# Optimization experiments

Hardware: AMD Instinct MI355X
Metric: run time of the kernel (lower is better)

The kernel has to match this reference:

```python
import jax, jax.numpy as jnp
import numpy as np

EMBED_DIM = 1024
NUM_HEADS = 16
HEAD_DIM = EMBED_DIM // NUM_HEADS


def setup_inputs() -> dict:
    key = jax.random.key(0)
    ks = jax.random.split(key, 9)
    B, T, D = 4, 2048, EMBED_DIM
    s = 1.0 / np.sqrt(D)
    inp = {
        "x": jax.random.normal(ks[0], (B, T, D), dtype=jnp.float32),
        "Wq": jax.random.normal(ks[1], (D, D), dtype=jnp.float32) * s,
        "bq": jnp.zeros((D,), dtype=jnp.float32),
        "Wk": jax.random.normal(ks[2], (D, D), dtype=jnp.float32) * s,
        "bk": jnp.zeros((D,), dtype=jnp.float32),
        "Wv": jax.random.normal(ks[3], (D, D), dtype=jnp.float32) * s,
        "bv": jnp.zeros((D,), dtype=jnp.float32),
        "Wo": jax.random.normal(ks[4], (D, D), dtype=jnp.float32) * s,
        "bo": jnp.zeros((D,), dtype=jnp.float32),
    }
    return inp


def _attn(x, Wq, bq, Wk, bk, Wv, bv, Wo, bo):
    B, T, D = x.shape
    H, Hd = NUM_HEADS, HEAD_DIM
    # projections: Linear uses y = x @ W^T + b; here W stored as (D, D) acting as W^T already
    q = (x @ Wq + bq).reshape(B, T, H, Hd).transpose(0, 2, 1, 3)  # [B,H,T,Hd]
    k = (x @ Wk + bk).reshape(B, T, H, Hd).transpose(0, 2, 1, 3)
    v = (x @ Wv + bv).reshape(B, T, H, Hd).transpose(0, 2, 1, 3)
    scores = jnp.einsum("bhqd,bhkd->bhqk", q, k) / np.sqrt(Hd)  # [B,H,T,T]
    causal = jnp.tril(jnp.ones((T, T), dtype=bool))
    scores = jnp.where(causal, scores, -jnp.inf)
    w = jax.nn.softmax(scores, axis=-1)
    out = jnp.einsum("bhqk,bhkd->bhqd", w, v)  # [B,H,T,Hd]
    out = out.transpose(0, 2, 1, 3).reshape(B, T, D)
    return out @ Wo + bo


def reference(x, Wq, bq, Wk, bk, Wv, bv, Wo, bo):
    return _attn(x, Wq, bq, Wk, bk, Wv, bv, Wo, bo)
```

## Files before the change

### kernel.cpp

```cpp
#include <hip/hip_runtime.h>
#include <cstdint>
#include <cstddef>

#define DI __device__ __forceinline__

typedef unsigned short u16;
typedef short bf16x8 __attribute__((ext_vector_type(8)));
typedef unsigned short u16x8 __attribute__((ext_vector_type(8)));
typedef float f32x4 __attribute__((ext_vector_type(4)));

static constexpr int DMODEL = 1024, T = 2048, BB = 4, NH = 16, HD = 64;
static constexpr int M = BB * T;

static constexpr size_t XB_OFF = 0;
static constexpr size_t WT_OFF = (size_t)M * DMODEL;
static constexpr size_t Q_OFF  = WT_OFF + 4ull * DMODEL * DMODEL;
static constexpr size_t K_OFF  = Q_OFF + (size_t)M * DMODEL;
static constexpr size_t V_OFF  = K_OFF + (size_t)M * DMODEL;
static constexpr size_t O_OFF  = XB_OFF;

DI u16 f2bf(float x) {
  unsigned int u = __builtin_bit_cast(unsigned int, x);
  u += 0x7fffu + ((u >> 16) & 1u);
  return (u16)(u >> 16);
}

DI unsigned int cvtpk_bf16(float a, float b) {
  unsigned int r;
  asm("v_cvt_pk_bf16_f32 %0, %1, %2" : "=v"(r) : "v"(a), "v"(b));
  return r;
}

DI void gld_lds16(const void* g, void* l) {
  __builtin_amdgcn_global_load_lds(
      (const __attribute__((address_space(1))) void*)g,
      (__attribute__((address_space(3))) void*)l, 16, 0, 0);
}

__global__ void k_cast(const float* __restrict__ in, u16* __restrict__ out) {
  size_t i = (size_t)(blockIdx.x * 256 + threadIdx.x) * 8;
  float4 a = *(const float4*)(in + i);
  float4 b = *(const float4*)(in + i + 4);
  u16x8 v;
  v[0] = f2bf(a.x); v[1] = f2bf(a.y); v[2] = f2bf(a.z); v[3] = f2bf(a.w);
  v[4] = f2bf(b.x); v[5] = f2bf(b.y); v[6] = f2bf(b.z); v[7] = f2bf(b.w);
  *(u16x8*)(out + i) = v;
}

__global__ void k_transw(const float* __restrict__ Wq, const float* __restrict__ Wk,
                         const float* __restrict__ Wv, const float* __restrict__ Wo,
                         u16* __restrict__ WtBase) {
  __shared__ u16 tile[32][33];
  const int z = blockIdx.z;
  const float* W = z == 0 ? Wq : (z == 1 ? Wk : (z == 2 ? Wv : Wo));
  u16* Wt = WtBase + (size_t)z * DMODEL * DMODEL;
  int tx = threadIdx.x, ty = threadIdx.y;
  int c = blockIdx.x * 32 + tx;
#pragma unroll
  for (int i = 0; i < 4; ++i) {
    int r = blockIdx.y * 32 + ty + i * 8;
    tile[ty + i * 8][tx] = f2bf(W[(size_t)r * DMODEL + c]);
  }
  __syncthreads();
#pragma unroll
  for (int i = 0; i < 4; ++i) {
    int rw = blockIdx.x * 32 + ty + i * 8;
    Wt[(size_t)rw * DMODEL + blockIdx.y * 32 + tx] = tile[tx][ty + i * 8];
  }
}

__launch_bounds__(256, 2)
__global__ void k_gemm_qkv(const u16* __restrict__ A, const u16* __restrict__ Wt,
                           const float* __restrict__ bq, const float* __restrict__ bk,
                           const float* __restrict__ bv,
                           u16* __restrict__ Qo, u16* __restrict__ Ko, u16* __restrict__ Vo) {
  __shared__ u16 As[128 * 64];
  __shared__ u16 Bs[128 * 64];
  const int z = blockIdx.z;
  const u16* Bt = Wt + (size_t)z * DMODEL * DMODEL;
  const float* bias = z == 0 ? bq : (z == 1 ? bk : bv);
  u16* out = z == 0 ? Qo : (z == 1 ? Ko : Vo);
  const float scale = z == 0 ? 0.125f * 1.4426950408889634f : 1.0f;

  const int tid = threadIdx.x;
  const int wave = tid >> 6, lane = tid & 63;
  const int g = lane >> 4, l15 = lane & 15;
  const int brow = blockIdx.x * 128, bcol = blockIdx.y * 128;
  const int wr = wave >> 1, wc = wave & 1;
  const int srow = tid >> 3, schunk = tid & 7;

  f32x4 acc[4][4] = {};

  for (int k0 = 0; k0 < DMODEL; k0 += 64) {
    __syncthreads();
#pragma unroll
    for (int j = 0; j < 4; ++j) {
      int r = j * 32 + srow;
      int cs = (schunk ^ (r & 7)) * 8;
      gld_lds16(A + (size_t)(brow + r) * DMODEL + k0 + cs, (char*)As + j * 4096 + wave * 1024);
      gld_lds16(Bt + (size_t)(bcol + r) * DMODEL + k0 + cs, (char*)Bs + j * 4096 + wave * 1024);
    }
    __syncthreads();
#pragma unroll
    for (int kh = 0; kh < 2; ++kh) {
      bf16x8 af[4], bfr[4];
#pragma unroll
      for (int m = 0; m < 4; ++m) {
        int r = wr * 64 + m * 16 + l15;
        int ch = (kh * 4 + g) ^ (r & 7);
        af[m] = *(const bf16x8*)((const char*)As + r * 128 + ch * 16);
      }
#pragma unroll
      for (int n = 0; n < 4; ++n) {
        int r = wc * 64 + n * 16 + l15;
        int ch = (kh * 4 + g) ^ (r & 7);
        bfr[n] = *(const bf16x8*)((const char*)Bs + r * 128 + ch * 16);
      }
#pragma unroll
      for (int m = 0; m < 4; ++m)
#pragma unroll
        for (int n = 0; n < 4; ++n)
          acc[m][n] = __builtin_amdgcn_mfma_f32_16x16x32_bf16(af[m], bfr[n], acc[m][n], 0, 0, 0);
    }
  }

#pragma unroll
  for (int m = 0; m < 4; ++m)
#pragma unroll
    for (int n = 0; n < 4; ++n) {
      int col = bcol + wc * 64 + n * 16 + l15;
      float bias_v = bias[col];
      int h = col >> 6, d = col & 63;
#pragma unroll
      for (int r = 0; r < 4; ++r) {
        int row = brow + wr * 64 + m * 16 + g * 4 + r;
        int b = row >> 11, t = row & 2047;
        float v = (acc[m][n][r] + bias_v) * scale;
        out[(((size_t)(b * NH + h) * T + t) << 6) + d] = f2bf(v);
      }
    }
}

__launch_bounds__(256, 2)
__global__ void k_gemm_out(const u16* __restrict__ A, const u16* __restrict__ Bt,
                           const float* __restrict__ bias, float* __restrict__ out) {
  __shared__ u16 As[128 * 64];
  __shared__ u16 Bs[128 * 64];
  const int tid = threadIdx.x;
  const int wave = tid >> 6, lane = tid & 63;
  const int g = lane >> 4, l15 = lane & 15;
  const int brow = blockIdx.x * 128, bcol = blockIdx.y * 128;
  const int wr = wave >> 1, wc = wave & 1;
  const int srow = tid >> 3, schunk = tid & 7;

  f32x4 acc[4][4] = {};

  for (int k0 = 0; k0 < DMODEL; k0 += 64) {
    __syncthreads();
#pragma unroll
    for (int j = 0; j < 4; ++j) {
      int r = j * 32 + srow;
      int cs = (schunk ^ (r & 7)) * 8;
      gld_lds16(A + (size_t)(brow + r) * DMODEL + k0 + cs, (char*)As + j * 4096 + wave * 1024);
      gld_lds16(Bt + (size_t)(bcol + r) * DMODEL + k0 + cs, (char*)Bs + j * 4096 + wave * 1024);
    }
    __syncthreads();
#pragma unroll
    for (int kh = 0; kh < 2; ++kh) {
      bf16x8 af[4], bfr[4];
#pragma unroll
      for (int m = 0; m < 4; ++m) {
        int r = wr * 64 + m * 16 + l15;
        int ch = (kh * 4 + g) ^ (r & 7);
        af[m] = *(const bf16x8*)((const char*)As + r * 128 + ch * 16);
      }
#pragma unroll
      for (int n = 0; n < 4; ++n) {
        int r = wc * 64 + n * 16 + l15;
        int ch = (kh * 4 + g) ^ (r & 7);
        bfr[n] = *(const bf16x8*)((const char*)Bs + r * 128 + ch * 16);
      }
#pragma unroll
      for (int m = 0; m < 4; ++m)
#pragma unroll
        for (int n = 0; n < 4; ++n)
          acc[m][n] = __builtin_amdgcn_mfma_f32_16x16x32_bf16(af[m], bfr[n], acc[m][n], 0, 0, 0);
    }
  }

#pragma unroll
  for (int m = 0; m < 4; ++m)
#pragma unroll
    for (int n = 0; n < 4; ++n) {
      int col = bcol + wc * 64 + n * 16 + l15;
      float bias_v = bias[col];
#pragma unroll
      for (int r = 0; r < 4; ++r) {
        int row = brow + wr * 64 + m * 16 + g * 4 + r;
        out[(size_t)row * DMODEL + col] = acc[m][n][r] + bias_v;
      }
    }
}

__launch_bounds__(256, 4)
__global__ void k_attn(const u16* __restrict__ Qw, const u16* __restrict__ Kw,
                       const u16* __restrict__ Vw, u16* __restrict__ Ow) {
  __shared__ u16 Ks[2][64 * 64];
  __shared__ u16 Vt[2][64 * 64];
  __shared__ u16 Ot[64 * 64];

  const int tid = threadIdx.x;
  const int wave = tid >> 6, lane = tid & 63;
  const int g = lane >> 4, l15 = lane & 15;
  const int tl = (l15 & 3) | ((l15 & 4) << 1) | ((l15 & 8) >> 1);
  const int qp = blockIdx.x;
  const int bh = blockIdx.y;
  const u16* Qb = Qw + (size_t)bh * T * HD;
  const u16* Kb = Kw + (size_t)bh * T * HD;
  const u16* Vb = Vw + (size_t)bh * T * HD;
  const int b = bh >> 4, h = bh & 15;
  const int vp = tid & 31, vcg = tid >> 5;
  const int krow = tid >> 3, kchunk = tid & 7;

  for (int half = 0; half < 2; ++half) {
    const int qt = half == 0 ? (31 - qp) : qp;
    const int ntiles = qt + 1;

    bf16x8 qf[2];
    {
      int qrow = qt * 64 + wave * 16 + l15;
#pragma unroll
      for (int kh = 0; kh < 2; ++kh)
        qf[kh] = *(const bf16x8*)(Qb + (size_t)qrow * HD + kh * 32 + g * 8);
    }

    f32x4 oacc[4] = {};
    float mrun = -1e30f, lrun = 0.f;

#pragma unroll
    for (int j = 0; j < 2; ++j) {
      int r = j * 32 + krow;
      gld_lds16(Kb + (size_t)r * HD + (kchunk ^ (r & 7)) * 8,
                (char*)(Ks[0]) + j * 4096 + wave * 1024);
    }
    {
      const u16* gv = Vb + (size_t)(2 * vp) * HD + vcg * 8;
      bf16x8 v0 = *(const bf16x8*)gv;
      bf16x8 v1 = *(const bf16x8*)(gv + HD);
      char* vtb = (char*)(Vt[0]);
#pragma unroll
      for (int j = 0; j < 8; ++j) {
        int c = vcg * 8 + j;
        int byteoff = (c * 128 + 4 * vp) ^ ((c & 7) << 4);
        unsigned int pk = (unsigned int)(u16)v0[j] | ((unsigned int)(u16)v1[j] << 16);
        *(unsigned int*)(vtb + byteoff) = pk;
      }
    }

    for (int kt = 0; kt < ntiles; ++kt) {
      __syncthreads();
      const int cur = kt & 1;
      const bool havenext = (kt + 1 < ntiles);

      if (havenext) {
#pragma unroll
        for (int j = 0; j < 2; ++j) {
          int r = j * 32 + krow;
          gld_lds16(Kb + (size_t)((kt + 1) * 64 + r) * HD + (kchunk ^ (r & 7)) * 8,
                    (char*)(Ks[cur ^ 1]) + j * 4096 + wave * 1024);
        }
      }
      bf16x8 v0, v1;
      if (havenext) {
        const u16* gv = Vb + (size_t)((kt + 1) * 64 + 2 * vp) * HD + vcg * 8;
        v0 = *(const bf16x8*)gv;
        v1 = *(const bf16x8*)(gv + HD);
      }

      bf16x8 kf[2][4];
#pragma unroll
      for (int kh = 0; kh < 2; ++kh)
#pragma unroll
        for (int n = 0; n < 4; ++n) {
          int rr = n * 16 + tl;
          int ch = (kh * 4 + g) ^ (rr & 7);
          kf[kh][n] = *(const bf16x8*)((const char*)(Ks[cur]) + rr * 128 + ch * 16);
        }

      f32x4 s[4] = {};
#pragma unroll
      for (int kh = 0; kh < 2; ++kh)
#pragma unroll
        for (int n = 0; n < 4; ++n)
          s[n] = __builtin_amdgcn_mfma_f32_16x16x32_bf16(kf[kh][n], qf[kh], s[n], 0, 0, 0);

      if (kt == qt) {
        int q_in = wave * 16 + l15;
#pragma unroll
        for (int n = 0; n < 4; ++n)
#pragma unroll
          for (int r = 0; r < 4; ++r) {
            int kv_in = n * 16 + (g & 1) * 8 + (g >> 1) * 4 + r;
            if (kv_in > q_in) s[n][r] = -1e30f;
          }
      }

      float vmax = s[0][0];
#pragma unroll
      for (int n = 0; n < 4; ++n)
#pragma unroll
        for (int r = 0; r < 4; ++r) vmax = fmaxf(vmax, s[n][r]);
      vmax = fmaxf(vmax, __shfl_xor(vmax, 16));
      vmax = fmaxf(vmax, __shfl_xor(vmax, 32));
      float mnew = fmaxf(mrun, vmax);
      float a = exp2f(mrun - mnew);
      mrun = mnew;
      float ps = 0.f;
#pragma unroll
      for (int n = 0; n < 4; ++n)
#pragma unroll
        for (int r = 0; r < 4; ++r) {
          float p = exp2f(s[n][r] - mnew);
          s[n][r] = p;
          ps += p;
        }
      ps += __shfl_xor(ps, 16);
      ps += __shfl_xor(ps, 32);
      lrun = lrun * a + ps;
#pragma unroll
      for (int n = 0; n < 4; ++n)
#pragma unroll
        for (int r = 0; r < 4; ++r) oacc[n][r] *= a;

#pragma unroll
      for (int kvh = 0; kvh < 2; ++kvh) {
        const int nlo = kvh * 2, nhi = kvh * 2 + 1;
        unsigned int L0 = cvtpk_bf16(s[nlo][0], s[nlo][1]);
        unsigned int L1 = cvtpk_bf16(s[nlo][2], s[nlo][3]);
        unsigned int H0 = cvtpk_bf16(s[nhi][0], s[nhi][1]);
        unsigned int H1 = cvtpk_bf16(s[nhi][2], s[nhi][3]);
        asm volatile("v_permlane32_swap_b32 %0, %1" : "+v"(L0), "+v"(H0));
        asm volatile("v_permlane32_swap_b32 %0, %1" : "+v"(L1), "+v"(H1));
        bf16x8 pb;
        unsigned int* pw = (unsigned int*)&pb;
        pw[0] = L0; pw[1] = L1; pw[2] = H0; pw[3] = H1;

        const int ch = ((kvh * 4 + g) ^ (l15 & 7)) * 16;
#pragma unroll
        for (int n = 0; n < 4; ++n) {
          bf16x8 an = *(const bf16x8*)((const char*)(Vt[cur]) + (n * 16 + l15) * 128 + ch);
          oacc[n] = __builtin_amdgcn_mfma_f32_16x16x32_bf16(an, pb, oacc[n], 0, 0, 0);
        }
      }

      if (havenext) {
        char* vtb = (char*)(Vt[cur ^ 1]);
#pragma unroll
        for (int j = 0; j < 8; ++j) {
          int c = vcg * 8 + j;
          int byteoff = (c * 128 + 4 * vp) ^ ((c & 7) << 4);
          unsigned int pk = (unsigned int)(u16)v0[j] | ((unsigned int)(u16)v1[j] << 16);
          *(unsigned int*)(vtb + byteoff) = pk;
        }
      }
    }

    {
      float inv = 1.f / lrun;
      char* otb = (char*)Ot;
#pragma unroll
      for (int n = 0; n < 4; ++n)
#pragma unroll
        for (int i = 0; i < 2; ++i) {
          unsigned int w = cvtpk_bf16(oacc[n][2 * i] * inv, oacc[n][2 * i + 1] * inv);
          int didx = n * 8 + g * 2 + i;
          int off = (wave * 16 + l15) * 128 + ((didx * 4) ^ ((l15 & 7) << 4));
          *(unsigned int*)(otb + off) = w;
        }
      __syncthreads();
      int q = tid >> 2, seg = tid & 3;
      uint4 c0 = *(const uint4*)(otb + q * 128 + (((seg * 2) ^ (q & 7)) << 4));
      uint4 c1 = *(const uint4*)(otb + q * 128 + (((seg * 2 + 1) ^ (q & 7)) << 4));
      u16* dst = Ow + ((size_t)b * T + qt * 64 + q) * DMODEL + h * 64 + seg * 16;
      *(uint4*)dst = c0;
      *(uint4*)(dst + 8) = c1;
    }
  }
}

extern "C" void kernel_launch(void* const* d_in, const int* in_sizes, int n_in,
                              void* d_out, int out_size, void* d_ws, size_t ws_size,
                              hipStream_t stream) {
  const float* x  = (const float*)d_in[0];
  const float* Wq = (const float*)d_in[1];
  const float* bq = (const float*)d_in[2];
  const float* Wk = (const float*)d_in[3];
  const float* bk = (const float*)d_in[4];
  const float* Wv = (const float*)d_in[5];
  const float* bv = (const float*)d_in[6];
  const float* Wo = (const float*)d_in[7];
  const float* bo = (const float*)d_in[8];
  float* out = (float*)d_out;
  u16* ws = (u16*)d_ws;

  k_cast<<<4096, 256, 0, stream>>>(x, ws + XB_OFF);
  k_transw<<<dim3(32, 32, 4), dim3(32, 8), 0, stream>>>(Wq, Wk, Wv, Wo, ws + WT_OFF);
  k_gemm_qkv<<<dim3(64, 8, 3), 256, 0, stream>>>(ws + XB_OFF, ws + WT_OFF, bq, bk, bv,
                                                 ws + Q_OFF, ws + K_OFF, ws + V_OFF);
  k_attn<<<dim3(16, 64), 256, 0, stream>>>(ws + Q_OFF, ws + K_OFF, ws + V_OFF, ws + O_OFF);
  k_gemm_out<<<dim3(64, 8), 256, 0, stream>>>(ws + O_OFF, ws + WT_OFF + 3ull * DMODEL * DMODEL,
                                              bo, out);
}
```

Baseline: 175.5 us.

## Reuse K LDS for output staging, add lazy softmax rescale and MFMA priority

The attention kernel drops its separate output staging buffer and reuses the K tile LDS instead, adding barriers around that reuse, and raises the launch-bounds occupancy hint from 4 to 5. Online-softmax rescaling of the accumulator is skipped unless some lane's running max grows by more than 8 (log2 units). Other changes: s_setprio around the MFMA blocks, a tree-shaped max reduction, byte-permute packing for the V transpose, and reordered prefetch issue. The aim is more resident waves and less VALU work per tile, at the cost of extra barriers, register pressure from the tighter bound, and dependence on the lazy-rescale threshold for numerical safety.

Measured after the change: 193.6 us. +10.4%, slower.

```diff
diff --git a/kernel.cpp b/kernel.cpp
--- a/kernel.cpp
+++ b/kernel.cpp
@@ -202,12 +202,11 @@
     }
 }
 
-__launch_bounds__(256, 4)
+__launch_bounds__(256, 5)
 __global__ void k_attn(const u16* __restrict__ Qw, const u16* __restrict__ Kw,
                        const u16* __restrict__ Vw, u16* __restrict__ Ow) {
   __shared__ u16 Ks[2][64 * 64];
   __shared__ u16 Vt[2][64 * 64];
-  __shared__ u16 Ot[64 * 64];
 
   const int tid = threadIdx.x;
   const int wave = tid >> 6, lane = tid & 63;
@@ -237,23 +236,26 @@
     f32x4 oacc[4] = {};
     float mrun = -1e30f, lrun = 0.f;
 
-#pragma unroll
-    for (int j = 0; j < 2; ++j) {
-      int r = j * 32 + krow;
-      gld_lds16(Kb + (size_t)r * HD + (kchunk ^ (r & 7)) * 8,
-                (char*)(Ks[0]) + j * 4096 + wave * 1024);
-    }
     {
       const u16* gv = Vb + (size_t)(2 * vp) * HD + vcg * 8;
       bf16x8 v0 = *(const bf16x8*)gv;
       bf16x8 v1 = *(const bf16x8*)(gv + HD);
+#pragma unroll
+      for (int j = 0; j < 2; ++j) {
+        int r = j * 32 + krow;
+        gld_lds16(Kb + (size_t)r * HD + (kchunk ^ (r & 7)) * 8,
+                  (char*)(Ks[0]) + j * 4096 + wave * 1024);
+      }
       char* vtb = (char*)(Vt[0]);
-#pragma unroll
-      for (int j = 0; j < 8; ++j) {
-        int c = vcg * 8 + j;
-        int byteoff = (c * 128 + 4 * vp) ^ ((c & 7) << 4);
-        unsigned int pk = (unsigned int)(u16)v0[j] | ((unsigned int)(u16)v1[j] << 16);
-        *(unsigned int*)(vtb + byteoff) = pk;
+      const unsigned int* w0 = (const unsigned int*)&v0;
+      const unsigned int* w1 = (const unsigned int*)&v1;
+#pragma unroll
+      for (int d2 = 0; d2 < 4; ++d2) {
+        int c0 = vcg * 8 + 2 * d2, c1 = c0 + 1;
+        unsigned int pk0 = __builtin_amdgcn_perm(w1[d2], w0[d2], 0x05040100u);
+        unsigned int pk1 = __builtin_amdgcn_perm(w1[d2], w0[d2], 0x07060302u);
+        *(unsigned int*)(vtb + ((c0 * 128 + 4 * vp) ^ ((c0 & 7) << 4))) = pk0;
+        *(unsigned int*)(vtb + ((c1 * 128 + 4 * vp) ^ ((c1 & 7) << 4))) = pk1;
       }
     }
 
@@ -262,19 +264,17 @@
       const int cur = kt & 1;
       const bool havenext = (kt + 1 < ntiles);
 
-      if (havenext) {
-#pragma unroll
-        for (int j = 0; j < 2; ++j) {
-          int r = j * 32 + krow;
-          gld_lds16(Kb + (size_t)((kt + 1) * 64 + r) * HD + (kchunk ^ (r & 7)) * 8,
-                    (char*)(Ks[cur ^ 1]) + j * 4096 + wave * 1024);
-        }
-      }
       bf16x8 v0, v1;
       if (havenext) {
         const u16* gv = Vb + (size_t)((kt + 1) * 64 + 2 * vp) * HD + vcg * 8;
         v0 = *(const bf16x8*)gv;
         v1 = *(const bf16x8*)(gv + HD);
+#pragma unroll
+        for (int j = 0; j < 2; ++j) {
+          int r = j * 32 + krow;
+          gld_lds16(Kb + (size_t)((kt + 1) * 64 + r) * HD + (kchunk ^ (r & 7)) * 8,
+                    (char*)(Ks[cur ^ 1]) + j * 4096 + wave * 1024);
+        }
       }
 
       bf16x8 kf[2][4];
@@ -288,11 +288,13 @@
         }
 
       f32x4 s[4] = {};
+      __builtin_amdgcn_s_setprio(1);
 #pragma unroll
       for (int kh = 0; kh < 2; ++kh)
 #pragma unroll
         for (int n = 0; n < 4; ++n)
           s[n] = __builtin_amdgcn_mfma_f32_16x16x32_bf16(kf[kh][n], qf[kh], s[n], 0, 0, 0);
+      __builtin_amdgcn_s_setprio(0);
 
       if (kt == qt) {
         int q_in = wave * 16 + l15;
@@ -305,33 +307,40 @@
           }
       }
 
-      float vmax = s[0][0];
-#pragma unroll
-      for (int n = 0; n < 4; ++n)
-#pragma unroll
-        for (int r = 0; r < 4; ++r) vmax = fmaxf(vmax, s[n][r]);
+      float t0 = fmaxf(fmaxf(s[0][0], s[0][1]), s[0][2]);
+      float t1 = fmaxf(fmaxf(s[0][3], s[1][0]), s[1][1]);
+      float t2 = fmaxf(fmaxf(s[1][2], s[1][3]), s[2][0]);
+      float t3 = fmaxf(fmaxf(s[2][1], s[2][2]), s[2][3]);
+      float t4 = fmaxf(fmaxf(s[3][0], s[3][1]), s[3][2]);
+      float vmax = fmaxf(fmaxf(fmaxf(t0, t1), t2), fmaxf(fmaxf(t3, t4), s[3][3]));
       vmax = fmaxf(vmax, __shfl_xor(vmax, 16));
       vmax = fmaxf(vmax, __shfl_xor(vmax, 32));
-      float mnew = fmaxf(mrun, vmax);
-      float a = exp2f(mrun - mnew);
-      mrun = mnew;
+
+      if (!__all(vmax - mrun <= 8.f)) {
+        float mnew = fmaxf(mrun, vmax);
+        float a = exp2f(mrun - mnew);
+        lrun *= a;
+#pragma unroll
+        for (int n = 0; n < 4; ++n)
+#pragma unroll
+          for (int r = 0; r < 4; ++r) oacc[n][r] *= a;
+        mrun = mnew;
+      }
+
       float ps = 0.f;
 #pragma unroll
       for (int n = 0; n < 4; ++n)
 #pragma unroll
         for (int r = 0; r < 4; ++r) {
-          float p = exp2f(s[n][r] - mnew);
+          float p = exp2f(s[n][r] - mrun);
           s[n][r] = p;
           ps += p;
         }
       ps += __shfl_xor(ps, 16);
       ps += __shfl_xor(ps, 32);
-      lrun = lrun * a + ps;
-#pragma unroll
-      for (int n = 0; n < 4; ++n)
-#pragma unroll
-        for (int r = 0; r < 4; ++r) oacc[n][r] *= a;
-
+      lrun += ps;
+
+      __builtin_amdgcn_s_setprio(1);
 #pragma unroll
       for (int kvh = 0; kvh < 2; ++kvh) {
         const int nlo = kvh * 2, nhi = kvh * 2 + 1;
@@ -352,22 +361,27 @@
           oacc[n] = __builtin_amdgcn_mfma_f32_16x16x32_bf16(an, pb, oacc[n], 0, 0, 0);
         }
       }
+      __builtin_amdgcn_s_setprio(0);
 
       if (havenext) {
         char* vtb = (char*)(Vt[cur ^ 1]);
-#pragma unroll
-        for (int j = 0; j < 8; ++j) {
-          int c = vcg * 8 + j;
-          int byteoff = (c * 128 + 4 * vp) ^ ((c & 7) << 4);
-          unsigned int pk = (unsigned int)(u16)v0[j] | ((unsigned int)(u16)v1[j] << 16);
-          *(unsigned int*)(vtb + byteoff) = pk;
+        const unsigned int* w0 = (const unsigned int*)&v0;
+        const unsigned int* w1 = (const unsigned int*)&v1;
+#pragma unroll
+        for (int d2 = 0; d2 < 4; ++d2) {
+          int c0 = vcg * 8 + 2 * d2, c1 = c0 + 1;
+          unsigned int pk0 = __builtin_amdgcn_perm(w1[d2], w0[d2], 0x05040100u);
+          unsigned int pk1 = __builtin_amdgcn_perm(w1[d2], w0[d2], 0x07060302u);
+          *(unsigned int*)(vtb + ((c0 * 128 + 4 * vp) ^ ((c0 & 7) << 4))) = pk0;
+          *(unsigned int*)(vtb + ((c1 * 128 + 4 * vp) ^ ((c1 & 7) << 4))) = pk1;
         }
       }
     }
 
     {
+      __syncthreads();
       float inv = 1.f / lrun;
-      char* otb = (char*)Ot;
+      char* otb = (char*)Ks;
 #pragma unroll
       for (int n = 0; n < 4; ++n)
 #pragma unroll
@@ -384,6 +398,7 @@
       u16* dst = Ow + ((size_t)b * T + qt * 64 + q) * DMODEL + h * 64 + seg * 16;
       *(uint4*)dst = c0;
       *(uint4*)(dst + 8) = c1;
+      __syncthreads();
     }
   }
 }
```
